# Kernel optimization log

Hardware: AMD Instinct MI355X
Metric: run time of the kernel (lower is better)

Reference implementation:

```python
import jax, jax.numpy as jnp
import numpy as np

EPS = 1e-7  # keras backend.epsilon()
NUM_ROUTING = 3


def squash(v, axis=-1):
    s2 = jnp.sum(jnp.square(v), axis=axis, keepdims=True)
    scale = s2 / (1.0 + s2) / jnp.sqrt(s2 + EPS)
    return scale * v


def setup_inputs() -> dict:
    key = jax.random.key(0)
    k1, k2 = jax.random.split(key)
    B, J, I, P, Q = 64, 32, 2048, 32, 16
    inputs = jax.random.normal(k1, (B, I, Q), dtype=jnp.float32)
    # glorot_uniform for W [J, I, P, Q]
    fan_in, fan_out = Q, P
    limit = np.sqrt(6.0 / (fan_in + fan_out))
    W = jax.random.uniform(k2, (J, I, P, Q), dtype=jnp.float32, minval=-limit, maxval=limit)
    return {"inputs": inputs, "W": W}


def reference(inputs, W):
    # prediction vectors: u_hat[b,j,i,p] = sum_q inputs[b,i,q] * W[j,i,p,q]
    inputs_hat = jnp.einsum('biq,jipq->bjip', inputs, W)  # [B,J,I,P]
    inputs_hat_stop = jax.lax.stop_gradient(inputs_hat)
    B, J, I, _ = inputs_hat.shape
    b = jnp.zeros((B, J, I), dtype=inputs_hat.dtype)
    for _ in range(NUM_ROUTING - 1):
        c = jax.nn.softmax(b, axis=1)  # softmax over output capsules j
        v = squash(jnp.einsum('bji,bjip->bjp', c, inputs_hat_stop))
        b = b + jnp.einsum('bjp,bjip->bji', v, inputs_hat_stop)
    c = jax.nn.softmax(b, axis=1)
    return squash(jnp.einsum('bji,bjip->bjp', c, inputs_hat))  # [B,J,P]
```

## Files before the change

kernel.cpp:

```cpp
#include <hip/hip_runtime.h>


namespace {

using bfrag = __attribute__((ext_vector_type(8))) short;
using ffrag = __attribute__((ext_vector_type(4))) float;

constexpr int I_DIM = 2048;
constexpr int B_DIM = 64;
constexpr int N_DIM = 1024;
constexpr int TI    = 16;
constexpr int NIT   = I_DIM / TI;

__device__ __forceinline__ unsigned short f2bf(float f) {
    unsigned int u = __float_as_uint(f);
    return (unsigned short)((u + 0x7fffu + ((u >> 16) & 1u)) >> 16);
}

template<int CTRL>
__device__ __forceinline__ float dppf(float x) {
    return __int_as_float(
        __builtin_amdgcn_update_dpp(0, __float_as_int(x), CTRL, 0xF, 0xF, true));
}
__device__ __forceinline__ float sum16(float x) {
    x += dppf<0x121>(x); x += dppf<0x122>(x);
    x += dppf<0x124>(x); x += dppf<0x128>(x);
    return x;
}


__global__ __launch_bounds__(256)
void conv_w(const float* __restrict__ W, unsigned short* __restrict__ Wt) {
    const int t = blockIdx.x * 256 + threadIdx.x;
    const int i = t >> 10, n = t & 1023;
    const float* src = W + ((((n >> 5) * I_DIM + i) * 32 + (n & 31)) << 4);
    unsigned int o[8];
    #pragma unroll
    for (int k = 0; k < 8; ++k)
        o[k] = (unsigned int)f2bf(src[2 * k]) | ((unsigned int)f2bf(src[2 * k + 1]) << 16);
    uint4* d0 = reinterpret_cast<uint4*>(Wt + (((size_t)i * 2 + 0) * 1024 + n) * 8);
    uint4* d1 = reinterpret_cast<uint4*>(Wt + (((size_t)i * 2 + 1) * 1024 + n) * 8);
    *d0 = make_uint4(o[0], o[1], o[2], o[3]);
    *d1 = make_uint4(o[4], o[5], o[6], o[7]);
}

__global__ __launch_bounds__(256)
void conv_x(const float* __restrict__ x, unsigned short* __restrict__ xT2) {
    const int t = blockIdx.x * 256 + threadIdx.x;
    const int i = t >> 6, b = t & 63;
    const float* src = x + (((size_t)b * I_DIM + i) << 4);
    unsigned int o[16];
    #pragma unroll
    for (int k = 0; k < 8; ++k) {
        const float f0 = src[2 * k], f1 = src[2 * k + 1];
        const unsigned short h0 = f2bf(f0), h1 = f2bf(f1);
        const float l0 = f0 - __uint_as_float(((unsigned int)h0) << 16);
        const float l1 = f1 - __uint_as_float(((unsigned int)h1) << 16);
        o[k]     = (unsigned int)h0       | ((unsigned int)h1 << 16);
        o[8 + k] = (unsigned int)f2bf(l0) | ((unsigned int)f2bf(l1) << 16);
    }
    #pragma unroll
    for (int g = 0; g < 4; ++g) {
        uint4* dst = reinterpret_cast<uint4*>(xT2 + (((size_t)i * 4 + g) * 64 + b) * 8);
        *dst = make_uint4(o[4 * g], o[4 * g + 1], o[4 * g + 2], o[4 * g + 3]);
    }
}

template<int MODE>
__global__ __launch_bounds__(256, 4)
void caps_sweep(const unsigned short* __restrict__ Wt,
                const unsigned short* __restrict__ xT2,
                const float* __restrict__ v_in,
                const float* __restrict__ c_in,
                float* __restrict__ d_out,
                float* __restrict__ sp_out)
{
    const int tid = threadIdx.x;
    const int w  = tid >> 6;
    const int l  = tid & 63;
    const int g  = l >> 4;
    const int li = l & 15;

    const int bid = (int)blockIdx.x;
    const int V   = ((bid & 7) << 7) | (bid >> 3);
    const int it  = ((V >> 7) << 4) | ((V & 127) >> 3);
    const int jg  = V & 7;
    const int j   = (jg << 2) + w;
    const int i0  = it << 4;
    const int ilast = i0 + TI - 1;

    const int aoff = ((g << 6) + li) << 3;
    const int boff = ((((g & 1) << 10) + (j << 5) + li)) << 3;

    float vr[4][4][2];
    if (MODE == 1) {
        #pragma unroll
        for (int bg = 0; bg < 4; ++bg)
            #pragma unroll
            for (int r = 0; r < 4; ++r)
                #pragma unroll
                for (int t = 0; t < 2; ++t)
                    vr[bg][r][t] = v_in[((((bg << 4) + (g << 2) + r) << 5) + j) * 32
                                        + (t << 4) + li];
    }

    ffrag s[4][2];
    #pragma unroll
    for (int bg = 0; bg < 4; ++bg) {
        s[bg][0] = ffrag{0.f, 0.f, 0.f, 0.f};
        s[bg][1] = ffrag{0.f, 0.f, 0.f, 0.f};
    }

    bfrag A0[4], B0[2], A1[4], B1[2];

    auto loadf = [&](int i, bfrag (&A)[4], bfrag (&B)[2]) {
        const unsigned short* xa = xT2 + (size_t)i * 2048 + aoff;
        #pragma unroll
        for (int bg = 0; bg < 4; ++bg)
            A[bg] = *reinterpret_cast<const bfrag*>(xa + (bg << 7));
        const unsigned short* xb = Wt + (size_t)i * 16384 + boff;
        B[0] = *reinterpret_cast<const bfrag*>(xb);
        B[1] = *reinterpret_cast<const bfrag*>(xb + 128);
    };

    loadf(i0, A0, B0);

    auto body = [&](int i, bfrag (&CA)[4], bfrag (&CB)[2],
                    bfrag (&NA)[4], bfrag (&NB)[2]) {
        ffrag c4[4];
        if (MODE == 2) {
            const float* cb = c_in + ((size_t)i << 11) + (j << 6) + (g << 2);
            #pragma unroll
            for (int bg = 0; bg < 4; ++bg)
                c4[bg] = *reinterpret_cast<const ffrag*>(cb + (bg << 4));
        }
        const int inx = (i < ilast) ? i + 1 : i;
        loadf(inx, NA, NB);
        asm volatile("" ::: "memory");

        #pragma unroll
        for (int bg = 0; bg < 4; ++bg) {
            if (MODE == 0) {
                s[bg][0] = __builtin_amdgcn_mfma_f32_16x16x32_bf16(CA[bg], CB[0], s[bg][0], 0, 0, 0);
                s[bg][1] = __builtin_amdgcn_mfma_f32_16x16x32_bf16(CA[bg], CB[1], s[bg][1], 0, 0, 0);
            } else {
                const ffrag z{0.f, 0.f, 0.f, 0.f};
                const ffrag u0 = __builtin_amdgcn_mfma_f32_16x16x32_bf16(CA[bg], CB[0], z, 0, 0, 0);
                const ffrag u1 = __builtin_amdgcn_mfma_f32_16x16x32_bf16(CA[bg], CB[1], z, 0, 0, 0);
                if (MODE == 1) {
                    float d0 = sum16(u0[0] * vr[bg][0][0] + u1[0] * vr[bg][0][1]);
                    float d1 = sum16(u0[1] * vr[bg][1][0] + u1[1] * vr[bg][1][1]);
                    float d2 = sum16(u0[2] * vr[bg][2][0] + u1[2] * vr[bg][2][1]);
                    float d3 = sum16(u0[3] * vr[bg][3][0] + u1[3] * vr[bg][3][1]);
                    float sel = d0;
                    sel = (li == 1) ? d1 : sel;
                    sel = (li == 2) ? d2 : sel;
                    sel = (li == 3) ? d3 : sel;
                    if (li < 4)
                        d_out[((size_t)i << 11) + (j << 6) + (bg << 4) + (g << 2) + li] = sel;
                } else {
                    #pragma unroll
                    for (int r = 0; r < 4; ++r) {
                        s[bg][0][r] += c4[bg][r] * u0[r];
                        s[bg][1][r] += c4[bg][r] * u1[r];
                    }
                }
            }
        }
    };

    for (int cc = 0; cc < TI / 2; ++cc) {
        body(i0 + 2 * cc,     A0, B0, A1, B1);
        body(i0 + 2 * cc + 1, A1, B1, A0, B0);
    }

    if (MODE != 1) {
        const float sc = (MODE == 0) ? (1.f / 32.f) : 1.f;
        #pragma unroll
        for (int bg = 0; bg < 4; ++bg)
            #pragma unroll
            for (int t = 0; t < 2; ++t)
                #pragma unroll
                for (int r = 0; r < 4; ++r)
                    sp_out[((size_t)((it << 6) + (bg << 4) + (g << 2) + r) << 10)
                           + (j << 5) + (t << 4) + li] = s[bg][t][r] * sc;
    }
}

__global__ __launch_bounds__(256)
void softmax_dc(const float* __restrict__ d, float* __restrict__ c) {
    const int t = blockIdx.x * 256 + threadIdx.x;
    const int i = t >> 6, b = t & 63;
    const float* dp = d + ((size_t)i << 11) + b;
    float v[32];
    float m = -1e30f;
    #pragma unroll
    for (int jx = 0; jx < 32; ++jx) { v[jx] = dp[jx << 6]; m = fmaxf(m, v[jx]); }
    float sm = 0.f;
    #pragma unroll
    for (int jx = 0; jx < 32; ++jx) { v[jx] = __expf(v[jx] - m); sm += v[jx]; }
    const float inv = 1.f / sm;
    float* cp = c + ((size_t)i << 11) + b;
    #pragma unroll
    for (int jx = 0; jx < 32; ++jx) cp[jx << 6] = v[jx] * inv;
}

__global__ __launch_bounds__(256)
void squash_reduce(const float* __restrict__ s_part,
                   const float* __restrict__ base,
                   float* __restrict__ dst) {
    const int tid = threadIdx.x;
    const int rr  = blockIdx.x * 8 + (tid >> 5);
    const int p   = tid & 31;
    const int b   = rr >> 5, jx = rr & 31;
    const float* sp = s_part + (size_t)b * N_DIM + (jx << 5) + p;
    float a0 = 0.f, a1 = 0.f, a2 = 0.f, a3 = 0.f;
    for (int it2 = 0; it2 < NIT; it2 += 4) {
        a0 += sp[(size_t)(it2 + 0) << 16];
        a1 += sp[(size_t)(it2 + 1) << 16];
        a2 += sp[(size_t)(it2 + 2) << 16];
        a3 += sp[(size_t)(it2 + 3) << 16];
    }
    const float sv = (a0 + a1) + (a2 + a3);
    float n2 = sv * sv;
    n2 = sum16(n2);
    n2 += __shfl_xor(n2, 16);
    const float scl = n2 / ((1.f + n2) * sqrtf(n2 + 1e-7f));
    dst[rr * 32 + p] = (base ? base[rr * 32 + p] : 0.f) + scl * sv;
}

}

extern "C" void kernel_launch(void* const* d_in, const int* in_sizes, int n_in,
                              void* d_out, int out_size, void* d_ws, size_t ws_size,
                              hipStream_t stream) {
    const float* x = (const float*)d_in[0];
    const float* W = (const float*)d_in[1];
    float* out = (float*)d_out;

    const size_t needW = (size_t)I_DIM * 2 * 1024 * 8 * 2;
    const size_t needX = (size_t)I_DIM * 4 * 64 * 8 * 2;
    const size_t needD = (size_t)I_DIM * 32 * 64 * 4;
    const size_t needP = (size_t)NIT * B_DIM * N_DIM * 4;
    const size_t needV = (size_t)B_DIM * N_DIM * 4;

    char* pp = (char*)d_ws;
    unsigned short* Wt  = (unsigned short*)pp; pp += needW;
    unsigned short* xT2 = (unsigned short*)pp; pp += needX;
    float* dbuf   = (float*)pp; pp += needD;
    float* cbuf   = (float*)pp; pp += needD;
    float* s_part = (float*)pp; pp += needP;
    float* v1     = (float*)pp; pp += needV;
    float* vs     = (float*)pp;
    (void)ws_size;

    conv_x<<<(I_DIM * B_DIM) / 256, 256, 0, stream>>>(x, xT2);
    conv_w<<<(I_DIM * N_DIM) / 256, 256, 0, stream>>>(W, Wt);

    const dim3 rg(1024), rb(256);
    const dim3 sg(512), sb(256);
    const dim3 qg(256), qb(256);

    caps_sweep<0><<<rg, rb, 0, stream>>>(Wt, xT2, nullptr, nullptr, nullptr, s_part);
    squash_reduce<<<qg, qb, 0, stream>>>(s_part, nullptr, v1);

    caps_sweep<1><<<rg, rb, 0, stream>>>(Wt, xT2, v1, nullptr, dbuf, nullptr);
    softmax_dc<<<sg, sb, 0, stream>>>(dbuf, cbuf);
    caps_sweep<2><<<rg, rb, 0, stream>>>(Wt, xT2, nullptr, cbuf, nullptr, s_part);
    squash_reduce<<<qg, qb, 0, stream>>>(s_part, v1, vs);

    caps_sweep<1><<<rg, rb, 0, stream>>>(Wt, xT2, vs, nullptr, dbuf, nullptr);
    softmax_dc<<<sg, sb, 0, stream>>>(dbuf, cbuf);
    caps_sweep<2><<<rg, rb, 0, stream>>>(Wt, xT2, nullptr, cbuf, nullptr, s_part);
    squash_reduce<<<qg, qb, 0, stream>>>(s_part, nullptr, out);
}
```

Measured before the change: 280.5 us.

## Deepen operand prefetch to two iterations and pack routing vectors as bf16

```diff
diff --git a/kernel.cpp b/kernel.cpp
--- a/kernel.cpp
+++ b/kernel.cpp
@@ -16,6 +16,13 @@
     unsigned int u = __float_as_uint(f);
     return (unsigned short)((u + 0x7fffu + ((u >> 16) & 1u)) >> 16);
 }
+__device__ __forceinline__ unsigned int cvtpk(float lo, float hi) {
+    unsigned int r;
+    asm("v_cvt_pk_bf16_f32 %0, %1, %2" : "=v"(r) : "v"(lo), "v"(hi));
+    return r;
+}
+__device__ __forceinline__ float bflo(unsigned int u) { return __uint_as_float(u << 16); }
+__device__ __forceinline__ float bfhi(unsigned int u) { return __uint_as_float(u & 0xffff0000u); }
 
 template<int CTRL>
 __device__ __forceinline__ float dppf(float x) {
@@ -87,21 +94,19 @@
     const int jg  = V & 7;
     const int j   = (jg << 2) + w;
     const int i0  = it << 4;
-    const int ilast = i0 + TI - 1;
 
     const int aoff = ((g << 6) + li) << 3;
     const int boff = ((((g & 1) << 10) + (j << 5) + li)) << 3;
 
-    float vr[4][4][2];
+    unsigned int vr[4][4];
     if (MODE == 1) {
         #pragma unroll
         for (int bg = 0; bg < 4; ++bg)
             #pragma unroll
-            for (int r = 0; r < 4; ++r)
-                #pragma unroll
-                for (int t = 0; t < 2; ++t)
-                    vr[bg][r][t] = v_in[((((bg << 4) + (g << 2) + r) << 5) + j) * 32
-                                        + (t << 4) + li];
+            for (int r = 0; r < 4; ++r) {
+                const float* vp = v_in + ((((bg << 4) + (g << 2) + r) << 5) + j) * 32;
+                vr[bg][r] = cvtpk(vp[li], vp[li + 16]);
+            }
     }
 
     ffrag s[4][2];
@@ -111,67 +116,91 @@
         s[bg][1] = ffrag{0.f, 0.f, 0.f, 0.f};
     }
 
+    const unsigned short* pa = xT2 + (size_t)i0 * 2048 + aoff;
+    const unsigned short* pb = Wt + (size_t)i0 * 16384 + boff;
+
     bfrag A0[4], B0[2], A1[4], B1[2];
-
-    auto loadf = [&](int i, bfrag (&A)[4], bfrag (&B)[2]) {
-        const unsigned short* xa = xT2 + (size_t)i * 2048 + aoff;
-        #pragma unroll
-        for (int bg = 0; bg < 4; ++bg)
-            A[bg] = *reinterpret_cast<const bfrag*>(xa + (bg << 7));
-        const unsigned short* xb = Wt + (size_t)i * 16384 + boff;
-        B[0] = *reinterpret_cast<const bfrag*>(xb);
-        B[1] = *reinterpret_cast<const bfrag*>(xb + 128);
-    };
-
-    loadf(i0, A0, B0);
+    #pragma unroll
+    for (int bg = 0; bg < 4; ++bg) {
+        A0[bg] = *reinterpret_cast<const bfrag*>(pa + (bg << 7));
+        A1[bg] = *reinterpret_cast<const bfrag*>(pa + 2048 + (bg << 7));
+    }
+    B0[0] = *reinterpret_cast<const bfrag*>(pb);
+    B0[1] = *reinterpret_cast<const bfrag*>(pb + 128);
+    B1[0] = *reinterpret_cast<const bfrag*>(pb + 16384);
+    B1[1] = *reinterpret_cast<const bfrag*>(pb + 16384 + 128);
 
     auto body = [&](int i, bfrag (&CA)[4], bfrag (&CB)[2],
-                    bfrag (&NA)[4], bfrag (&NB)[2]) {
-        ffrag c4[4];
-        if (MODE == 2) {
+                    int offA, int offB) {
+        if (MODE == 0) {
+            #pragma unroll
+            for (int bg = 0; bg < 4; ++bg) {
+                s[bg][0] = __builtin_amdgcn_mfma_f32_16x16x32_bf16(CA[bg], CB[0], s[bg][0], 0, 0, 0);
+                s[bg][1] = __builtin_amdgcn_mfma_f32_16x16x32_bf16(CA[bg], CB[1], s[bg][1], 0, 0, 0);
+            }
+            #pragma unroll
+            for (int bg = 0; bg < 4; ++bg)
+                CA[bg] = *reinterpret_cast<const bfrag*>(pa + offA + (bg << 7));
+            CB[0] = *reinterpret_cast<const bfrag*>(pb + offB);
+            CB[1] = *reinterpret_cast<const bfrag*>(pb + offB + 128);
+        } else if (MODE == 1) {
+            const ffrag z{0.f, 0.f, 0.f, 0.f};
+            ffrag u0[4], u1[4];
+            #pragma unroll
+            for (int bg = 0; bg < 4; ++bg) {
+                u0[bg] = __builtin_amdgcn_mfma_f32_16x16x32_bf16(CA[bg], CB[0], z, 0, 0, 0);
+                u1[bg] = __builtin_amdgcn_mfma_f32_16x16x32_bf16(CA[bg], CB[1], z, 0, 0, 0);
+            }
+            #pragma unroll
+            for (int bg = 0; bg < 4; ++bg)
+                CA[bg] = *reinterpret_cast<const bfrag*>(pa + offA + (bg << 7));
+            CB[0] = *reinterpret_cast<const bfrag*>(pb + offB);
+            CB[1] = *reinterpret_cast<const bfrag*>(pb + offB + 128);
+
+            #pragma unroll
+            for (int bg = 0; bg < 4; ++bg) {
+                float d0 = sum16(u0[bg][0] * bflo(vr[bg][0]) + u1[bg][0] * bfhi(vr[bg][0]));
+                float d1 = sum16(u0[bg][1] * bflo(vr[bg][1]) + u1[bg][1] * bfhi(vr[bg][1]));
+                float d2 = sum16(u0[bg][2] * bflo(vr[bg][2]) + u1[bg][2] * bfhi(vr[bg][2]));
+                float d3 = sum16(u0[bg][3] * bflo(vr[bg][3]) + u1[bg][3] * bfhi(vr[bg][3]));
+                float sel = d0;
+                sel = (li == 1) ? d1 : sel;
+                sel = (li == 2) ? d2 : sel;
+                sel = (li == 3) ? d3 : sel;
+                if (li < 4)
+                    d_out[((size_t)i << 11) + (j << 6) + (bg << 4) + (g << 2) + li] = sel;
+            }
+        } else {
+            ffrag c4[4];
             const float* cb = c_in + ((size_t)i << 11) + (j << 6) + (g << 2);
             #pragma unroll
             for (int bg = 0; bg < 4; ++bg)
                 c4[bg] = *reinterpret_cast<const ffrag*>(cb + (bg << 4));
-        }
-        const int inx = (i < ilast) ? i + 1 : i;
-        loadf(inx, NA, NB);
-        asm volatile("" ::: "memory");
-
-        #pragma unroll
-        for (int bg = 0; bg < 4; ++bg) {
-            if (MODE == 0) {
-                s[bg][0] = __builtin_amdgcn_mfma_f32_16x16x32_bf16(CA[bg], CB[0], s[bg][0], 0, 0, 0);
-                s[bg][1] = __builtin_amdgcn_mfma_f32_16x16x32_bf16(CA[bg], CB[1], s[bg][1], 0, 0, 0);
-            } else {
-                const ffrag z{0.f, 0.f, 0.f, 0.f};
+            const ffrag z{0.f, 0.f, 0.f, 0.f};
+            #pragma unroll
+            for (int bg = 0; bg < 4; ++bg) {
                 const ffrag u0 = __builtin_amdgcn_mfma_f32_16x16x32_bf16(CA[bg], CB[0], z, 0, 0, 0);
                 const ffrag u1 = __builtin_amdgcn_mfma_f32_16x16x32_bf16(CA[bg], CB[1], z, 0, 0, 0);
-                if (MODE == 1) {
-                    float d0 = sum16(u0[0] * vr[bg][0][0] + u1[0] * vr[bg][0][1]);
-                    float d1 = sum16(u0[1] * vr[bg][1][0] + u1[1] * vr[bg][1][1]);
-                    float d2 = sum16(u0[2] * vr[bg][2][0] + u1[2] * vr[bg][2][1]);
-                    float d3 = sum16(u0[3] * vr[bg][3][0] + u1[3] * vr[bg][3][1]);
-                    float sel = d0;
-                    sel = (li == 1) ? d1 : sel;
-                    sel = (li == 2) ? d2 : sel;
-                    sel = (li == 3) ? d3 : sel;
-                    if (li < 4)
-                        d_out[((size_t)i << 11) + (j << 6) + (bg << 4) + (g << 2) + li] = sel;
-                } else {
-                    #pragma unroll
-                    for (int r = 0; r < 4; ++r) {
-                        s[bg][0][r] += c4[bg][r] * u0[r];
-                        s[bg][1][r] += c4[bg][r] * u1[r];
-                    }
+                #pragma unroll
+                for (int r = 0; r < 4; ++r) {
+                    s[bg][0][r] += c4[bg][r] * u0[r];
+                    s[bg][1][r] += c4[bg][r] * u1[r];
                 }
             }
+            #pragma unroll
+            for (int bg = 0; bg < 4; ++bg)
+                CA[bg] = *reinterpret_cast<const bfrag*>(pa + offA + (bg << 7));
+            CB[0] = *reinterpret_cast<const bfrag*>(pb + offB);
+            CB[1] = *reinterpret_cast<const bfrag*>(pb + offB + 128);
         }
     };
 
     for (int cc = 0; cc < TI / 2; ++cc) {
-        body(i0 + 2 * cc,     A0, B0, A1, B1);
-        body(i0 + 2 * cc + 1, A1, B1, A0, B0);
+        const int i = i0 + 2 * cc;
+        body(i,     A0, B0, 2 * 2048, 2 * 16384);
+        body(i + 1, A1, B1, 3 * 2048, 3 * 16384);
+        pa += 2 * 2048;
+        pb += 2 * 16384;
     }
 
     if (MODE != 1) {
```

New measurement: 277.3 us. About the same (-1.2%).
